# Performance work log

Measured on AMD Instinct MI355X. Metric: run time of the kernel, lower is better.

Reference implementation:

```python
import jax, jax.numpy as jnp
import numpy as np

# Model dims
B = 64            # scenes (memory batch)
APER = 16         # agents per scene (uniform `length`)
A = B * APER      # total agents = sum(length)
TPAST = 20
TFUT = 30         # len_future
C = 256           # controller_size
M = 128           # memory_m
N = 256           # memory_n
H = 5             # num_heads (future modes)
SPACE = N // APER # per-agent write slot band
EMB = 16
D = C + M         # decoder hidden size


def _gru(x, h, wih, whh, bih, bhh):
    """torch.nn.GRU single-cell step."""
    gi = x @ wih.T + bih
    gh = h @ whh.T + bhh
    ir, iz, inn = jnp.split(gi, 3, axis=-1)
    hr, hz, hn = jnp.split(gh, 3, axis=-1)
    r = jax.nn.sigmoid(ir + hr)
    z = jax.nn.sigmoid(iz + hz)
    n = jnp.tanh(inn + r * hn)
    return (1.0 - z) * n + z * h


def _address(k, beta, mem, mask):
    """NTM content addressing: beta-sharpened masked softmax over cosine sims.
    k: (...,B,APER,M), beta: (...,B,APER,1), mem: (B,N,M), mask: (APER,N)."""
    kn = k / (jnp.linalg.norm(k, axis=-1, keepdims=True) + 1e-16)
    mn = mem / (jnp.linalg.norm(mem, axis=-1, keepdims=True) + 1e-16)
    sim = jnp.einsum('...bam,bnm->...ban', kn, mn)
    logits = beta * sim + (mask - 1.0) * 1e9
    return jax.nn.softmax(logits, axis=-1)


def setup_inputs() -> dict:
    key = jax.random.key(0)
    ks = iter(jax.random.split(key, 64))
    def nrm(shape, scale):
        return jax.random.normal(next(ks), shape, dtype=jnp.float32) * scale
    inp = dict(
        past=nrm((A, TPAST, 2), 1.0),
        past_rel=nrm((A, TPAST, 2), 1.0),
        ep_w1=nrm((8, 2), 0.7), ep_b1=jnp.zeros(8), ep_w2=nrm((EMB, 8), 0.35), ep_b2=jnp.zeros(EMB),
        er_w1=nrm((8, 2), 0.7), er_b1=jnp.zeros(8), er_w2=nrm((EMB, 8), 0.35), er_b2=jnp.zeros(EMB),
        enc_wih=nrm((3 * C, EMB + M), 1.0 / np.sqrt(EMB + M)), enc_whh=nrm((3 * C, C), 1.0 / np.sqrt(C)),
        enc_bih=jnp.zeros(3 * C), enc_bhh=jnp.zeros(3 * C),
        rel_wih=nrm((3 * C, EMB), 1.0 / np.sqrt(EMB)), rel_whh=nrm((3 * C, C), 1.0 / np.sqrt(C)),
        rel_bih=jnp.zeros(3 * C), rel_bhh=jnp.zeros(3 * C),
        dec_wih=nrm((3 * D, D), 1.0 / np.sqrt(D)), dec_whh=nrm((3 * D, D), 1.0 / np.sqrt(D)),
        dec_bih=jnp.zeros(3 * D), dec_bhh=jnp.zeros(3 * D),
        out_w=nrm((2, D), 1.0 / np.sqrt(D)), out_b=jnp.zeros(2),
        read_w=nrm((H, M + 1, C), 1.0 / np.sqrt(C)), read_b=jnp.zeros((H, M + 1)),
        write_w=nrm((3 * M + 1, C), 1.0 / np.sqrt(C)), write_b=jnp.zeros(3 * M + 1),
        init_r=nrm((1, M), 0.01),
        h_bias=nrm((1, C), 0.05), h_rel_bias=nrm((1, C), 0.05), h_fut_bias=nrm((1, D), 0.05),
        mem_bias=nrm((N, M), 0.05),
    )
    return inp


def reference(past, past_rel, ep_w1, ep_b1, ep_w2, ep_b2, er_w1, er_b1, er_w2, er_b2,
              enc_wih, enc_whh, enc_bih, enc_bhh, rel_wih, rel_whh, rel_bih, rel_bhh,
              dec_wih, dec_whh, dec_bih, dec_bhh, out_w, out_b,
              read_w, read_b, write_w, write_b,
              init_r, h_bias, h_rel_bias, h_fut_bias, mem_bias):
    # Per-agent disjoint write bands; read mask = other agents' bands.
    owner = jnp.arange(N) // SPACE
    mask_w = (owner[None, :] == jnp.arange(APER)[:, None]).astype(jnp.float32)  # (APER,N)
    mask_r = 1.0 - mask_w

    def mlp(x, w1, b1, w2, b2):
        return jax.nn.relu(x @ w1.T + b1) @ w2.T + b2

    emb_p = jnp.transpose(mlp(past, ep_w1, ep_b1, ep_w2, ep_b2), (1, 0, 2))      # (T,A,16)
    emb_r = jnp.transpose(mlp(past_rel, er_w1, er_b1, er_w2, er_b2), (1, 0, 2))  # (T,A,16)

    def step(carry, xs):
        emb, embr = xs
        mem, h, hr, hf, r = carry
        h = _gru(jnp.concatenate([emb, r], axis=-1), h, enc_wih, enc_whh, enc_bih, enc_bhh)
        hr = _gru(embr, hr, rel_wih, rel_whh, rel_bih, rel_bhh)
        # write head: k, beta, erase, add
        wp = h @ write_w.T + write_b
        kw = jnp.tanh(wp[:, :M]).reshape(B, APER, M)
        betaw = jax.nn.softplus(wp[:, M:M + 1]).reshape(B, APER, 1)
        er = jax.nn.sigmoid(wp[:, M + 1:2 * M + 1]).reshape(B, APER, M)
        ad = jnp.tanh(wp[:, 2 * M + 1:]).reshape(B, APER, M)
        ww = _address(kw, betaw, mem, mask_w)                                    # (B,APER,N)
        # erase/add; write bands are disjoint across agents so aggregation is exact
        mem = mem * (1.0 - jnp.einsum('ban,bam->bnm', ww, er)) + jnp.einsum('ban,bam->bnm', ww, ad)
        # per-head reads
        rp = jnp.einsum('ac,hkc->hak', hr, read_w) + read_b[:, None, :]          # (H,A,M+1)
        kr = jnp.tanh(rp[..., :M]).reshape(H, B, APER, M)
        betar = jax.nn.softplus(rp[..., M:]).reshape(H, B, APER, 1)
        wr = _address(kr, betar, mem, mask_r)                                    # (H,B,APER,N)
        reads = jnp.einsum('hban,bnm->hbam', wr, mem).reshape(H, A, M)
        r = reads[0]
        # per-mode decoder
        dec_in = jnp.concatenate([jnp.broadcast_to(h[None], (H, A, C)), reads], axis=-1).reshape(H * A, D)
        hf = _gru(dec_in, hf, dec_wih, dec_whh, dec_bih, dec_bhh)
        out = (hf @ out_w.T + out_b).reshape(H, A, 2)
        return (mem, h, hr, hf, r), out

    carry0 = (jnp.broadcast_to(mem_bias[None], (B, N, M)),
              jnp.broadcast_to(h_bias, (A, C)),
              jnp.broadcast_to(h_rel_bias, (A, C)),
              jnp.broadcast_to(h_fut_bias, (H * A, D)),
              jnp.broadcast_to(init_r, (A, M)))
    carry, _ = jax.lax.scan(step, carry0, (emb_p, emb_r))
    zf = jnp.zeros((TFUT, A, EMB), dtype=past.dtype)
    carry, outs = jax.lax.scan(step, carry, (zf, zf))                            # (TFUT,H,A,2)
    pred_rel = jnp.transpose(outs, (2, 1, 0, 3))                                 # (A,H,TFUT,2)
    pred = past[:, -1][:, None, None, :] + jnp.cumsum(pred_rel, axis=2)
    return pred, pred_rel
```

## Files before the change

kernel.cpp:

```cpp
#include <hip/hip_runtime.h>
#include <math.h>

#define B_    64
#define APER_ 16
#define A_    1024
#define TPAST_ 20
#define TFUT_  30
#define C_    256
#define M_    128
#define N_    256
#define H_    5
#define EMB_  16
#define D_    384
#define TTOT_ 50

typedef short bf16x8 __attribute__((ext_vector_type(8)));
typedef float f32x4 __attribute__((ext_vector_type(4)));

__device__ __forceinline__ float sigmoidf_(float x) { return 1.0f / (1.0f + expf(-x)); }
__device__ __forceinline__ float softplusf_(float x) { return (x > 20.0f) ? x : log1pf(expf(x)); }
__device__ __forceinline__ unsigned short f2bf(float f) {
    unsigned u = __float_as_uint(f);
    return (unsigned short)((u + 0x7FFFu + ((u >> 16) & 1u)) >> 16);
}
__device__ __forceinline__ float bf2f(short s) {
    return __uint_as_float(((unsigned)(unsigned short)s) << 16);
}

struct Cvt { const float* src; short* dst; int rows, sk, dk, total; };
struct Cvt8 { Cvt c[8]; };

__global__ __launch_bounds__(256) void convert_all(Cvt8 p)
{
    const int stride = gridDim.x * 256;
    #pragma unroll
    for (int s = 0; s < 8; ++s) {
        const Cvt d = p.c[s];
        for (int idx = blockIdx.x * 256 + threadIdx.x; idx < d.total; idx += stride) {
            const int r = idx / d.dk, k = idx % d.dk;
            float v = (k < d.sk && r < d.rows) ? d.src[(size_t)r * d.sk + k] : 0.f;
            d.dst[idx] = (short)f2bf(v);
        }
    }
}

__global__ __launch_bounds__(256) void embed2_k(const float* __restrict__ past, const float* __restrict__ past_rel,
                                                const float* __restrict__ pw1, const float* __restrict__ pb1,
                                                const float* __restrict__ pw2, const float* __restrict__ pb2,
                                                const float* __restrict__ rw1, const float* __restrict__ rb1,
                                                const float* __restrict__ rw2, const float* __restrict__ rb2,
                                                short* __restrict__ emb_p, short* __restrict__ emb_r)
{
    const int idx0 = blockIdx.x * 256 + threadIdx.x;
    const int half = A_ * TPAST_;
    if (idx0 >= 2 * half) return;
    const bool second = idx0 >= half;
    const int idx = second ? idx0 - half : idx0;
    const float* x = second ? past_rel : past;
    const float* w1 = second ? rw1 : pw1; const float* b1 = second ? rb1 : pb1;
    const float* w2 = second ? rw2 : pw2; const float* b2 = second ? rb2 : pb2;
    short* emb = second ? emb_r : emb_p;

    const int a = idx / TPAST_, t = idx % TPAST_;
    const float x0 = x[(size_t)idx * 2], x1 = x[(size_t)idx * 2 + 1];
    float hbuf[8];
    #pragma unroll
    for (int j = 0; j < 8; ++j) hbuf[j] = fmaxf(0.f, w1[j * 2] * x0 + w1[j * 2 + 1] * x1 + b1[j]);
    short* e = emb + ((size_t)t * A_ + a) * EMB_;
    #pragma unroll
    for (int i = 0; i < 16; ++i) {
        float acc = b2[i];
        #pragma unroll
        for (int j = 0; j < 8; ++j) acc += w2[i * 8 + j] * hbuf[j];
        e[i] = (short)f2bf(acc);
    }
}

__global__ __launch_bounds__(256) void init_k(float* __restrict__ h, const float* __restrict__ h_bias, short* __restrict__ hb,
                                              float* __restrict__ hr, const float* __restrict__ hr_bias, short* __restrict__ hrb,
                                              const float* __restrict__ hf_bias, short* __restrict__ hfb,
                                              short* __restrict__ reads_b, const float* __restrict__ init_r,
                                              float* __restrict__ mem, short* __restrict__ memhi, short* __restrict__ memlo,
                                              float* __restrict__ normsG, const float* __restrict__ mem_bias)
{
    const int idx = blockIdx.x * 256 + threadIdx.x;
    if (idx < B_ * N_ * M_) {
        const float v = mem_bias[idx & (N_ * M_ - 1)];
        mem[idx] = v;
        const short hv = (short)f2bf(v);
        memhi[idx] = hv;
        memlo[idx] = (short)f2bf(v - bf2f(hv));
    }
    if (idx < B_ * N_) {
        const float* r = mem_bias + (size_t)(idx & (N_ - 1)) * M_;
        float ss = 0.f;
        for (int k = 0; k < M_; ++k) ss += r[k] * r[k];
        normsG[idx] = sqrtf(ss) + 1e-16f;
    }
    if (idx < A_ * C_) {
        float v = h_bias[idx & (C_ - 1)];
        h[idx] = v; hb[idx] = (short)f2bf(v);
        v = hr_bias[idx & (C_ - 1)];
        hr[idx] = v; hrb[idx] = (short)f2bf(v);
    }
    if (idx < H_ * A_ * D_) {
        hfb[idx] = (short)f2bf(hf_bias[idx % D_]);
    }
    if (idx < A_ * M_) reads_b[idx] = (short)f2bf(init_r[idx & (M_ - 1)]);
}

__device__ __forceinline__ void gru_tile_split(
    int role, float* __restrict__ xchLane,
    const short* __restrict__ X1, int K1,
    const short* __restrict__ X2, int K2,
    const short* __restrict__ Wih, int Kpad,
    const float* __restrict__ bih,
    const short* __restrict__ Hb, const short* __restrict__ Whh,
    const float* __restrict__ bhh,
    const float* __restrict__ Hprev,
    float* __restrict__ Hnew, short* __restrict__ Hnewb,
    int G, int rowBase, int colBase, int lane)
{
    const int l16 = lane & 15;
    const int kb8 = (lane >> 4) * 8;
    const f32x4 z4 = {0.f, 0.f, 0.f, 0.f};
    f32x4 a0[2][2], a1[2][2], a2[2][2];
    #pragma unroll
    for (int i = 0; i < 2; ++i)
        #pragma unroll
        for (int j = 0; j < 2; ++j) { a0[i][j] = z4; a1[i][j] = z4; a2[i][j] = z4; }

    if (role == 0) {
        for (int kc = 0; kc < Kpad; kc += 32) {
            const int k8 = kc + kb8;
            bf16x8 ax[2];
            #pragma unroll
            for (int i = 0; i < 2; ++i) {
                const int r = rowBase + i * 16 + l16;
                bf16x8 v = {0, 0, 0, 0, 0, 0, 0, 0};
                if (k8 < K1) {
                    if (X1) v = *(const bf16x8*)(X1 + (size_t)(r & 1023) * K1 + k8);
                } else if (k8 < K1 + K2) {
                    v = *(const bf16x8*)(X2 + (size_t)r * K2 + (k8 - K1));
                }
                ax[i] = v;
            }
            #pragma unroll
            for (int j = 0; j < 2; ++j) {
                const size_t wb = (size_t)(colBase + j * 16 + l16) * Kpad + k8;
                const bf16x8 b0 = *(const bf16x8*)(Wih + wb);
                const bf16x8 b1 = *(const bf16x8*)(Wih + (size_t)G * Kpad + wb);
                const bf16x8 b2 = *(const bf16x8*)(Wih + (size_t)2 * G * Kpad + wb);
                a0[0][j] = __builtin_amdgcn_mfma_f32_16x16x32_bf16(ax[0], b0, a0[0][j], 0, 0, 0);
                a0[1][j] = __builtin_amdgcn_mfma_f32_16x16x32_bf16(ax[1], b0, a0[1][j], 0, 0, 0);
                a1[0][j] = __builtin_amdgcn_mfma_f32_16x16x32_bf16(ax[0], b1, a1[0][j], 0, 0, 0);
                a1[1][j] = __builtin_amdgcn_mfma_f32_16x16x32_bf16(ax[1], b1, a1[1][j], 0, 0, 0);
                a2[0][j] = __builtin_amdgcn_mfma_f32_16x16x32_bf16(ax[0], b2, a2[0][j], 0, 0, 0);
                a2[1][j] = __builtin_amdgcn_mfma_f32_16x16x32_bf16(ax[1], b2, a2[1][j], 0, 0, 0);
            }
        }
        #pragma unroll
        for (int i = 0; i < 2; ++i)
            #pragma unroll
            for (int j = 0; j < 2; ++j)
                #pragma unroll
                for (int q = 0; q < 4; ++q) {
                    const int base = (i * 2 + j) * 4 + q;
                    xchLane[base]      = a0[i][j][q];
                    xchLane[16 + base] = a1[i][j][q];
                    xchLane[32 + base] = a2[i][j][q];
                }
    } else {
        for (int kc = 0; kc < G; kc += 32) {
            const int k8 = kc + kb8;
            bf16x8 ah[2];
            #pragma unroll
            for (int i = 0; i < 2; ++i)
                ah[i] = *(const bf16x8*)(Hb + (size_t)(rowBase + i * 16 + l16) * G + k8);
            #pragma unroll
            for (int j = 0; j < 2; ++j) {
                const size_t wb = (size_t)(colBase + j * 16 + l16) * G + k8;
                const bf16x8 b0 = *(const bf16x8*)(Whh + wb);
                const bf16x8 b1 = *(const bf16x8*)(Whh + (size_t)G * G + wb);
                const bf16x8 b2 = *(const bf16x8*)(Whh + (size_t)2 * G * G + wb);
                a0[0][j] = __builtin_amdgcn_mfma_f32_16x16x32_bf16(ah[0], b0, a0[0][j], 0, 0, 0);
                a0[1][j] = __builtin_amdgcn_mfma_f32_16x16x32_bf16(ah[1], b0, a0[1][j], 0, 0, 0);
                a1[0][j] = __builtin_amdgcn_mfma_f32_16x16x32_bf16(ah[0], b1, a1[0][j], 0, 0, 0);
                a1[1][j] = __builtin_amdgcn_mfma_f32_16x16x32_bf16(ah[1], b1, a1[1][j], 0, 0, 0);
                a2[0][j] = __builtin_amdgcn_mfma_f32_16x16x32_bf16(ah[0], b2, a2[0][j], 0, 0, 0);
                a2[1][j] = __builtin_amdgcn_mfma_f32_16x16x32_bf16(ah[1], b2, a2[1][j], 0, 0, 0);
            }
        }
    }
    __syncthreads();
    if (role != 1) return;

    const int r4 = (lane >> 4) * 4;
    #pragma unroll
    for (int j = 0; j < 2; ++j) {
        const int col = colBase + j * 16 + l16;
        const float b0c = bih[col] + bhh[col];
        const float b1c = bih[G + col] + bhh[G + col];
        const float bi2 = bih[2 * G + col], bh2 = bhh[2 * G + col];
        #pragma unroll
        for (int i = 0; i < 2; ++i) {
            #pragma unroll
            for (int q = 0; q < 4; ++q) {
                const int row = rowBase + i * 16 + r4 + q;
                const int base = (i * 2 + j) * 4 + q;
                const float arv = a0[i][j][q] + xchLane[base];
                const float azv = a1[i][j][q] + xchLane[16 + base];
                const float aniv = xchLane[32 + base];
                const float anhv = a2[i][j][q];
                const float rr = sigmoidf_(arv + b0c);
                const float zz = sigmoidf_(azv + b1c);
                const float nn = tanhf(aniv + bi2 + rr * (anhv + bh2));
                const float hp = Hprev ? Hprev[(size_t)row * G + col]
                                       : bf2f(Hb[(size_t)row * G + col]);
                const float hv = (1.f - zz) * nn + zz * hp;
                if (Hnew) Hnew[(size_t)row * G + col] = hv;
                Hnewb[(size_t)row * G + col] = (short)f2bf(hv);
            }
        }
    }
}

__device__ __forceinline__ void gemm_tile(
    const short* __restrict__ Xb, const short* __restrict__ Wb,
    const float* __restrict__ bias, float* __restrict__ Out,
    int Ncols, int K, int rowBase, int colBase, int lane)
{
    const int l16 = lane & 15;
    const int kb8 = (lane >> 4) * 8;
    const f32x4 z4 = {0.f, 0.f, 0.f, 0.f};
    f32x4 acc[2][2] = {{z4, z4}, {z4, z4}};

    for (int kc = 0; kc < K; kc += 32) {
        const int k8 = kc + kb8;
        const bf16x8 a0 = *(const bf16x8*)(Xb + (size_t)(rowBase + l16) * K + k8);
        const bf16x8 a1 = *(const bf16x8*)(Xb + (size_t)(rowBase + 16 + l16) * K + k8);
        const bf16x8 b0 = *(const bf16x8*)(Wb + (size_t)(colBase + l16) * K + k8);
        const bf16x8 b1 = *(const bf16x8*)(Wb + (size_t)(colBase + 16 + l16) * K + k8);
        acc[0][0] = __builtin_amdgcn_mfma_f32_16x16x32_bf16(a0, b0, acc[0][0], 0, 0, 0);
        acc[0][1] = __builtin_amdgcn_mfma_f32_16x16x32_bf16(a0, b1, acc[0][1], 0, 0, 0);
        acc[1][0] = __builtin_amdgcn_mfma_f32_16x16x32_bf16(a1, b0, acc[1][0], 0, 0, 0);
        acc[1][1] = __builtin_amdgcn_mfma_f32_16x16x32_bf16(a1, b1, acc[1][1], 0, 0, 0);
    }
    const int r4 = (lane >> 4) * 4;
    #pragma unroll
    for (int j = 0; j < 2; ++j) {
        const int col = colBase + j * 16 + l16;
        if (col >= Ncols) continue;
        const float bv = bias[col];
        #pragma unroll
        for (int i = 0; i < 2; ++i)
            #pragma unroll
            for (int q = 0; q < 4; ++q) {
                const int row = rowBase + i * 16 + r4 + q;
                Out[(size_t)row * Ncols + col] = acc[i][j][q] + bv;
            }
    }
}

__global__ __launch_bounds__(256) void phaseA(
    const short* __restrict__ ep, const short* __restrict__ er,
    const short* __restrict__ enc_wih, const float* __restrict__ enc_bih,
    const short* __restrict__ enc_whh, const float* __restrict__ enc_bhh,
    const short* __restrict__ rel_wih, const float* __restrict__ rel_bih,
    const short* __restrict__ rel_whh, const float* __restrict__ rel_bhh,
    const short* __restrict__ dec_wih, const float* __restrict__ dec_bih,
    const short* __restrict__ dec_whh, const float* __restrict__ dec_bhh,
    const float* __restrict__ hc, const short* __restrict__ hbc,
    float* __restrict__ hn, short* __restrict__ hbn,
    const float* __restrict__ hrc, const short* __restrict__ hrbc,
    float* __restrict__ hrn, short* __restrict__ hrbn,
    const short* __restrict__ hfbc, short* __restrict__ hfbn,
    const short* __restrict__ reads_b,
    int decBlocks, int encBlocks)
{
    __shared__ float xch[2][64][49];
    const int bid = blockIdx.x;
    const int wv = threadIdx.x >> 6;
    const int lane = threadIdx.x & 63;
    const int pair = wv >> 1, role = wv & 1;
    float* xchLane = &xch[pair][lane][0];

    if (bid < decBlocks) {
        const int tile = bid * 2 + pair;
        gru_tile_split(role, xchLane,
                       hbc, 256, reads_b, 128, dec_wih, 384, dec_bih,
                       hfbc, dec_whh, dec_bhh, nullptr, nullptr, hfbn, D_,
                       (tile / 12) * 32, (tile % 12) * 32, lane);
    } else if (bid < decBlocks + encBlocks) {
        const int tile = (bid - decBlocks) * 2 + pair;
        gru_tile_split(role, xchLane,
                       ep, 16, reads_b, 128, enc_wih, 160, enc_bih,
                       hbc, enc_whh, enc_bhh, hc, hn, hbn, C_,
                       (tile >> 3) * 32, (tile & 7) * 32, lane);
    } else {
        const int tile = (bid - decBlocks - encBlocks) * 2 + pair;
        gru_tile_split(role, xchLane,
                       er, 16, nullptr, 0, rel_wih, 32, rel_bih,
                       hrbc, rel_whh, rel_bhh, hrc, hrn, hrbn, C_,
                       (tile >> 3) * 32, (tile & 7) * 32, lane);
    }
}

__global__ __launch_bounds__(256) void phaseHeads(
    const short* __restrict__ hbn, const short* __restrict__ write_w_b,
    const float* __restrict__ write_b, float* __restrict__ wp,
    const short* __restrict__ hrbn, const short* __restrict__ read_w_b,
    const float* __restrict__ read_b, float* __restrict__ rp,
    const short* __restrict__ hfbn, const float* __restrict__ out_w,
    const float* __restrict__ out_b, float* __restrict__ predrel,
    int outT, int wpBlocks, int rpBlocks)
{
    const int bid = blockIdx.x;
    const int wave = threadIdx.x >> 6;
    const int lane = threadIdx.x & 63;

    if (bid < wpBlocks) {
        const int tile = bid * 4 + wave;
        gemm_tile(hbn, write_w_b, write_b, wp, 385, C_,
                  (tile & 31) * 32, (tile >> 5) * 32, lane);
    } else if (bid < wpBlocks + rpBlocks) {
        const int tile = (bid - wpBlocks) * 4 + wave;
        gemm_tile(hrbn, read_w_b, read_b, rp, 645, C_,
                  (tile & 31) * 32, (tile >> 5) * 32, lane);
    } else {
        const int widx = (bid - wpBlocks - rpBlocks) * 4 + wave;
        const int g = lane >> 3, li = lane & 7;
        const int row = widx * 8 + g;
        const short* hrow = hfbn + (size_t)row * D_;
        float a0 = 0.f, a1 = 0.f;
        #pragma unroll
        for (int u = 0; u < 6; ++u) {
            const int k0 = u * 64 + li * 8;
            const bf16x8 v = *(const bf16x8*)(hrow + k0);
            #pragma unroll
            for (int r = 0; r < 8; ++r) {
                const float f = bf2f(v[r]);
                a0 = fmaf(f, out_w[k0 + r], a0);
                a1 = fmaf(f, out_w[D_ + k0 + r], a1);
            }
        }
        a0 += __shfl_xor(a0, 1); a0 += __shfl_xor(a0, 2); a0 += __shfl_xor(a0, 4);
        a1 += __shfl_xor(a1, 1); a1 += __shfl_xor(a1, 2); a1 += __shfl_xor(a1, 4);
        if (li == 0) {
            const int hh = row >> 10, aa = row & 1023;
            float* o = predrel + (((size_t)aa * H_ + hh) * TFUT_ + outT) * 2;
            o[0] = a0 + out_b[0];
            o[1] = a1 + out_b[1];
        }
    }
}

__global__ __launch_bounds__(256) void write_mem_k(const float* __restrict__ wp,
                                                   float* __restrict__ mem,
                                                   short* __restrict__ memhi, short* __restrict__ memlo,
                                                   float* __restrict__ normsG)
{
    const int a = blockIdx.x;
    const int b = a >> 4, p = a & 15;
    __shared__ float kw[128], er[128], ad[128], red[256], ww[16], logit[16];
    __shared__ float buf[2048];
    __shared__ float beta_s, knorm_s;
    const int tid = threadIdx.x;
    const float* w = wp + (size_t)a * 385;
    if (tid < 128) {
        kw[tid] = tanhf(w[tid]);
        er[tid] = sigmoidf_(w[129 + tid]);
        ad[tid] = tanhf(w[257 + tid]);
    }
    if (tid == 0) beta_s = softplusf_(w[128]);
    __syncthreads();

    red[tid] = (tid < 128) ? kw[tid] * kw[tid] : 0.f;
    __syncthreads();
    for (int s = 128; s > 0; s >>= 1) { if (tid < s) red[tid] += red[tid + s]; __syncthreads(); }
    if (tid == 0) knorm_s = sqrtf(red[0]) + 1e-16f;
    __syncthreads();

    const int s = tid >> 4, j = tid & 15;
    float dot = 0.f, ss = 0.f;
    {
        const float* mrow = mem + ((size_t)(b * N_) + p * 16 + s) * M_;
        for (int k = j; k < 128; k += 16) { float v = mrow[k]; dot += kw[k] * v; ss += v * v; }
    }
    red[tid] = dot; __syncthreads();
    for (int st = 8; st > 0; st >>= 1) { if (j < st) red[tid] += red[tid + st]; __syncthreads(); }
    float dotf = red[s * 16];
    __syncthreads();
    red[tid] = ss; __syncthreads();
    for (int st = 8; st > 0; st >>= 1) { if (j < st) red[tid] += red[tid + st]; __syncthreads(); }
    float ssf = red[s * 16];
    if (j == 0) {
        float mn = sqrtf(ssf) + 1e-16f;
        logit[s] = beta_s * (dotf / (mn * knorm_s));
    }
    __syncthreads();
    if (tid == 0) {
        float mx = -1e30f;
        for (int i = 0; i < 16; ++i) mx = fmaxf(mx, logit[i]);
        float sum = 0.f;
        for (int i = 0; i < 16; ++i) { float e = __expf(logit[i] - mx); ww[i] = e; sum += e; }
        float inv = 1.f / sum;
        for (int i = 0; i < 16; ++i) ww[i] *= inv;
    }
    __syncthreads();
    for (int idx = tid; idx < 16 * 128; idx += 256) {
        int si = idx >> 7, m = idx & 127;
        size_t g = ((size_t)(b * N_) + p * 16 + si) * M_ + m;
        float wwv = ww[si];
        float v = mem[g] * (1.f - wwv * er[m]) + wwv * ad[m];
        mem[g] = v;
        const short hv = (short)f2bf(v);
        memhi[g] = hv;
        memlo[g] = (short)f2bf(v - bf2f(hv));
        buf[idx] = v;
    }
    __syncthreads();
    {
        float ssq = 0.f;
        #pragma unroll
        for (int i = 0; i < 8; ++i) { float v = buf[s * 128 + j + 16 * i]; ssq += v * v; }
        #pragma unroll
        for (int m = 1; m < 16; m <<= 1) ssq += __shfl_xor(ssq, m);
        if (j == 0) normsG[b * N_ + p * 16 + s] = sqrtf(ssq) + 1e-16f;
    }
}

__global__ __launch_bounds__(256) void read_k2(const float* __restrict__ rp,
                                               const float* __restrict__ mem,
                                               const short* __restrict__ memhi,
                                               const short* __restrict__ memlo,
                                               const float* __restrict__ normsG,
                                               short* __restrict__ reads_b)
{
    const int b = blockIdx.x;
    const int h = blockIdx.y;
    __shared__ __align__(16) float kq[16 * 132];
    __shared__ float S[16 * 260];
    __shared__ float beta_s[16], knorm_s[16], inv_s[16];
    const int t = threadIdx.x;
    const int a = t >> 4;
    const int sub = t & 15;

    {
        const float* base = rp + ((size_t)(b * 16 + a)) * 645 + h * 129;
        const int k0 = sub * 8;
        float v[8]; float ss = 0.f;
        #pragma unroll
        for (int r = 0; r < 8; ++r) { v[r] = tanhf(base[k0 + r]); ss += v[r] * v[r]; }
        float* dst = kq + a * 132 + k0;
        *(float4*)dst = make_float4(v[0], v[1], v[2], v[3]);
        *(float4*)(dst + 4) = make_float4(v[4], v[5], v[6], v[7]);
        #pragma unroll
        for (int m = 1; m < 16; m <<= 1) ss += __shfl_xor(ss, m);
        if (sub == 0) {
            knorm_s[a] = sqrtf(ss) + 1e-16f;
            beta_s[a] = softplusf_(base[128]);
        }
    }
    __syncthreads();

    {
        const int wave = t >> 6, lane = t & 63;
        const int l16 = lane & 15, kb8 = (lane >> 4) * 8;
        const int slotBase = wave * 64;
        const f32x4 z4 = {0.f, 0.f, 0.f, 0.f};
        f32x4 acc[4] = {z4, z4, z4, z4};
        const short* mbh = memhi + (size_t)b * N_ * M_;
        const short* mbl = memlo + (size_t)b * N_ * M_;
        #pragma unroll
        for (int kc = 0; kc < 128; kc += 32) {
            const float* ap = kq + l16 * 132 + kc + kb8;
            bf16x8 ah, al;
            #pragma unroll
            for (int r = 0; r < 8; ++r) {
                const float av = ap[r];
                const short hv = (short)f2bf(av);
                ah[r] = hv; al[r] = (short)f2bf(av - bf2f(hv));
            }
            #pragma unroll
            for (int tt = 0; tt < 4; ++tt) {
                const size_t roff = (size_t)(slotBase + tt * 16 + l16) * M_ + kc + kb8;
                const bf16x8 bh = *(const bf16x8*)(mbh + roff);
                const bf16x8 bl = *(const bf16x8*)(mbl + roff);
                acc[tt] = __builtin_amdgcn_mfma_f32_16x16x32_bf16(ah, bh, acc[tt], 0, 0, 0);
                acc[tt] = __builtin_amdgcn_mfma_f32_16x16x32_bf16(ah, bl, acc[tt], 0, 0, 0);
                acc[tt] = __builtin_amdgcn_mfma_f32_16x16x32_bf16(al, bh, acc[tt], 0, 0, 0);
            }
        }
        const int r4 = (lane >> 4) * 4;
        #pragma unroll
        for (int tt = 0; tt < 4; ++tt) {
            const int slot = slotBase + tt * 16 + l16;
            const float nv = normsG[b * N_ + slot];
            #pragma unroll
            for (int q = 0; q < 4; ++q) {
                const int aq = r4 + q;
                const float lg = ((slot >> 4) == aq) ? -1e30f
                               : beta_s[aq] * acc[tt][q] / (nv * knorm_s[aq]);
                S[aq * 260 + slot] = lg;
            }
        }
    }
    __syncthreads();

    {
        float mx = -1e30f;
        #pragma unroll
        for (int i = 0; i < 16; ++i) mx = fmaxf(mx, S[a * 260 + sub + 16 * i]);
        #pragma unroll
        for (int m = 1; m < 16; m <<= 1) mx = fmaxf(mx, __shfl_xor(mx, m));
        float e[16]; float sum = 0.f;
        #pragma unroll
        for (int i = 0; i < 16; ++i) { e[i] = __expf(S[a * 260 + sub + 16 * i] - mx); sum += e[i]; }
        #pragma unroll
        for (int i = 0; i < 16; ++i) S[a * 260 + sub + 16 * i] = e[i];
        #pragma unroll
        for (int m = 1; m < 16; m <<= 1) sum += __shfl_xor(sum, m);
        if (sub == 0) inv_s[a] = 1.f / sum;
    }
    __syncthreads();

    {
        const int m0 = sub * 8;
        const float* mb = mem + (size_t)b * N_ * M_ + m0;
        float acc[8];
        #pragma unroll
        for (int r = 0; r < 8; ++r) acc[r] = 0.f;
        const float* Sa = S + a * 260;
        #pragma unroll 4
        for (int n = 0; n < N_; ++n) {
            const float w = Sa[n];
            const float4 v0 = *(const float4*)(mb + (size_t)n * M_);
            const float4 v1 = *(const float4*)(mb + (size_t)n * M_ + 4);
            acc[0] = fmaf(w, v0.x, acc[0]); acc[1] = fmaf(w, v0.y, acc[1]);
            acc[2] = fmaf(w, v0.z, acc[2]); acc[3] = fmaf(w, v0.w, acc[3]);
            acc[4] = fmaf(w, v1.x, acc[4]); acc[5] = fmaf(w, v1.y, acc[5]);
            acc[6] = fmaf(w, v1.z, acc[6]); acc[7] = fmaf(w, v1.w, acc[7]);
        }
        const float inv = inv_s[a];
        short pk[8];
        #pragma unroll
        for (int r = 0; r < 8; ++r) pk[r] = (short)f2bf(acc[r] * inv);
        *(bf16x8*)(reads_b + ((size_t)h * A_ + b * 16 + a) * M_ + m0) = *(bf16x8*)pk;
    }
}

__global__ __launch_bounds__(256) void cumsum_k(const float* __restrict__ past,
                                                const float* __restrict__ predrel,
                                                float* __restrict__ pred)
{
    const int idx = blockIdx.x * 256 + threadIdx.x;
    if (idx >= A_ * H_ * 2) return;
    const int c = idx & 1;
    const int ah = idx >> 1;
    const int a = ah / H_;
    float acc = past[((size_t)a * TPAST_ + TPAST_ - 1) * 2 + c];
    const float* pr = predrel + (size_t)ah * TFUT_ * 2 + c;
    float* pd = pred + (size_t)ah * TFUT_ * 2 + c;
    for (int t = 0; t < TFUT_; ++t) { acc += pr[t * 2]; pd[t * 2] = acc; }
}

extern "C" void kernel_launch(void* const* d_in, const int* in_sizes, int n_in,
                              void* d_out, int out_size, void* d_ws, size_t ws_size,
                              hipStream_t stream)
{
    const float* past       = (const float*)d_in[0];
    const float* past_rel   = (const float*)d_in[1];
    const float* ep_w1      = (const float*)d_in[2];
    const float* ep_b1      = (const float*)d_in[3];
    const float* ep_w2      = (const float*)d_in[4];
    const float* ep_b2      = (const float*)d_in[5];
    const float* er_w1      = (const float*)d_in[6];
    const float* er_b1      = (const float*)d_in[7];
    const float* er_w2      = (const float*)d_in[8];
    const float* er_b2      = (const float*)d_in[9];
    const float* enc_wih    = (const float*)d_in[10];
    const float* enc_whh    = (const float*)d_in[11];
    const float* enc_bih    = (const float*)d_in[12];
    const float* enc_bhh    = (const float*)d_in[13];
    const float* rel_wih    = (const float*)d_in[14];
    const float* rel_whh    = (const float*)d_in[15];
    const float* rel_bih    = (const float*)d_in[16];
    const float* rel_bhh    = (const float*)d_in[17];
    const float* dec_wih    = (const float*)d_in[18];
    const float* dec_whh    = (const float*)d_in[19];
    const float* dec_bih    = (const float*)d_in[20];
    const float* dec_bhh    = (const float*)d_in[21];
    const float* out_w      = (const float*)d_in[22];
    const float* out_b      = (const float*)d_in[23];
    const float* read_w     = (const float*)d_in[24];
    const float* read_b     = (const float*)d_in[25];
    const float* write_w    = (const float*)d_in[26];
    const float* write_b    = (const float*)d_in[27];
    const float* init_r     = (const float*)d_in[28];
    const float* h_bias     = (const float*)d_in[29];
    const float* h_rel_bias = (const float*)d_in[30];
    const float* h_fut_bias = (const float*)d_in[31];
    const float* mem_bias   = (const float*)d_in[32];

    float* pred    = (float*)d_out;
    float* predrel = pred + (size_t)A_ * H_ * TFUT_ * 2;

    float* ws = (float*)d_ws;
    size_t off = 0;
    auto alloc = [&](size_t n) { float* p = ws + off; off += n; return p; };
    float* h0     = alloc((size_t)A_ * C_);
    float* h1     = alloc((size_t)A_ * C_);
    float* hr0    = alloc((size_t)A_ * C_);
    float* hr1    = alloc((size_t)A_ * C_);
    float* mem    = alloc((size_t)B_ * N_ * M_);
    float* wp     = alloc((size_t)A_ * 385);
    float* rp     = alloc((size_t)A_ * 645);
    float* normsG = alloc((size_t)B_ * N_);

    short* sws = (short*)(ws + off);
    size_t soff = 0;
    auto salloc = [&](size_t n) { short* p = sws + soff; soff += n; return p; };
    short* emb_p_b   = salloc((size_t)TPAST_ * A_ * EMB_);
    short* emb_r_b   = salloc((size_t)TPAST_ * A_ * EMB_);
    short* hb0       = salloc((size_t)A_ * C_);
    short* hb1       = salloc((size_t)A_ * C_);
    short* hrb0      = salloc((size_t)A_ * C_);
    short* hrb1      = salloc((size_t)A_ * C_);
    short* hfb0      = salloc((size_t)H_ * A_ * D_);
    short* hfb1      = salloc((size_t)H_ * A_ * D_);
    short* reads_b   = salloc((size_t)H_ * A_ * M_);
    short* memhi     = salloc((size_t)B_ * N_ * M_);
    short* memlo     = salloc((size_t)B_ * N_ * M_);
    short* enc_wih_b = salloc((size_t)768 * 160);
    short* enc_whh_b = salloc((size_t)768 * 256);
    short* rel_wih_b = salloc((size_t)768 * 32);
    short* rel_whh_b = salloc((size_t)768 * 256);
    short* dec_wih_b = salloc((size_t)1152 * 384);
    short* dec_whh_b = salloc((size_t)1152 * 384);
    short* write_w_b = salloc((size_t)416 * 256);
    short* read_w_b  = salloc((size_t)672 * 256);
    (void)ws_size; (void)in_sizes; (void)n_in; (void)out_size;

    Cvt8 cp;
    cp.c[0] = {enc_wih, enc_wih_b, 768, 144, 160, 768 * 160};
    cp.c[1] = {enc_whh, enc_whh_b, 768, 256, 256, 768 * 256};
    cp.c[2] = {rel_wih, rel_wih_b, 768, 16, 32, 768 * 32};
    cp.c[3] = {rel_whh, rel_whh_b, 768, 256, 256, 768 * 256};
    cp.c[4] = {dec_wih, dec_wih_b, 1152, 384, 384, 1152 * 384};
    cp.c[5] = {dec_whh, dec_whh_b, 1152, 384, 384, 1152 * 384};
    cp.c[6] = {write_w, write_w_b, 385, 256, 256, 416 * 256};
    cp.c[7] = {read_w, read_w_b, 645, 256, 256, 672 * 256};
    convert_all<<<1024, 256, 0, stream>>>(cp);

    init_k<<<(B_ * N_ * M_ + 255) / 256, 256, 0, stream>>>(
        h0, h_bias, hb0, hr0, h_rel_bias, hrb0, h_fut_bias, hfb0,
        reads_b, init_r, mem, memhi, memlo, normsG, mem_bias);
    embed2_k<<<(2 * A_ * TPAST_ + 255) / 256, 256, 0, stream>>>(
        past, past_rel, ep_w1, ep_b1, ep_w2, ep_b2, er_w1, er_b1, er_w2, er_b2,
        emb_p_b, emb_r_b);

    float *hc = h0, *hn = h1, *hrc = hr0, *hrn = hr1;
    short *hbc = hb0, *hbn = hb1, *hrbc = hrb0, *hrbn = hrb1, *hfbc = hfb0, *hfbn = hfb1;

    const dim3 g_read(B_, H_);

    for (int t = 0; t < TTOT_; ++t) {
        const short* ep = (t < TPAST_) ? emb_p_b + (size_t)t * A_ * EMB_ : nullptr;
        const short* er = (t < TPAST_) ? emb_r_b + (size_t)t * A_ * EMB_ : nullptr;

        const int decBlocks = (t == 0) ? 0 : 960;
        phaseA<<<decBlocks + 256, 256, 0, stream>>>(
            ep, er,
            enc_wih_b, enc_bih, enc_whh_b, enc_bhh,
            rel_wih_b, rel_bih, rel_whh_b, rel_bhh,
            dec_wih_b, dec_bih, dec_whh_b, dec_bhh,
            hc, hbc, hn, hbn,
            hrc, hrbc, hrn, hrbn,
            hfbc, hfbn,
            reads_b, decBlocks, 128);

        const int gridH = (t >= 21) ? 432 : 272;
        phaseHeads<<<gridH, 256, 0, stream>>>(
            hbn, write_w_b, write_b, wp,
            hrbn, read_w_b, read_b, rp,
            hfbn, out_w, out_b, predrel, t - 21, 104, 168);

        write_mem_k<<<A_, 256, 0, stream>>>(wp, mem, memhi, memlo, normsG);

        read_k2<<<g_read, 256, 0, stream>>>(rp, mem, memhi, memlo, normsG, reads_b);

        float* tf; short* ts;
        tf = hc; hc = hn; hn = tf;       ts = hbc; hbc = hbn; hbn = ts;
        tf = hrc; hrc = hrn; hrn = tf;   ts = hrbc; hrbc = hrbn; hrbn = ts;
        if (t >= 1) {
            ts = hfbc; hfbc = hfbn; hfbn = ts;
        }
    }

    phaseA<<<960, 256, 0, stream>>>(
        nullptr, nullptr,
        enc_wih_b, enc_bih, enc_whh_b, enc_bhh,
        rel_wih_b, rel_bih, rel_whh_b, rel_bhh,
        dec_wih_b, dec_bih, dec_whh_b, dec_bhh,
        hc, hbc, hn, hbn,
        hrc, hrbc, hrn, hrbn,
        hfbc, hfbn,
        reads_b, 960, 0);
    phaseHeads<<<160, 256, 0, stream>>>(
        hbn, write_w_b, write_b, wp,
        hrbn, read_w_b, read_b, rp,
        hfbn, out_w, out_b, predrel, TFUT_ - 1, 0, 0);
    cumsum_k<<<(A_ * H_ * 2 + 255) / 256, 256, 0, stream>>>(past, predrel, pred);
}
```

Measured before the change: 6.146 ms.

## Fuse write-projection GEMM with memory write and drop fp32 memory copy

The write-head projection GEMM is folded into the memory-write step. Each of 64 per-scene blocks computes its 16 agents' write parameters into shared memory with MFMA, then applies the addressing softmax and erase/add update in place. The separate fp32 memory array is removed, and the hi/lo bf16 split pair becomes the only memory representation, read by both the write and read kernels. This removes one launch per step, the wp global round trip and the fp32 memory traffic. In exchange, the fused part runs on only 64 blocks with large shared-memory use, and values are reconstructed from the bf16 pairs on every access.

Result: slower. 6.653 ms (+8.2%).

```diff
diff --git a/kernel.cpp b/kernel.cpp
--- a/kernel.cpp
+++ b/kernel.cpp
@@ -80,13 +80,12 @@
                                               float* __restrict__ hr, const float* __restrict__ hr_bias, short* __restrict__ hrb,
                                               const float* __restrict__ hf_bias, short* __restrict__ hfb,
                                               short* __restrict__ reads_b, const float* __restrict__ init_r,
-                                              float* __restrict__ mem, short* __restrict__ memhi, short* __restrict__ memlo,
+                                              short* __restrict__ memhi, short* __restrict__ memlo,
                                               float* __restrict__ normsG, const float* __restrict__ mem_bias)
 {
     const int idx = blockIdx.x * 256 + threadIdx.x;
     if (idx < B_ * N_ * M_) {
         const float v = mem_bias[idx & (N_ * M_ - 1)];
-        mem[idx] = v;
         const short hv = (short)f2bf(v);
         memhi[idx] = hv;
         memlo[idx] = (short)f2bf(v - bf2f(hv));
@@ -306,29 +305,124 @@
     }
 }
 
-__global__ __launch_bounds__(256) void phaseHeads(
+__global__ __launch_bounds__(256) void phaseB(
     const short* __restrict__ hbn, const short* __restrict__ write_w_b,
-    const float* __restrict__ write_b, float* __restrict__ wp,
+    const float* __restrict__ write_b,
+    short* __restrict__ memhi, short* __restrict__ memlo,
+    float* __restrict__ normsG,
     const short* __restrict__ hrbn, const short* __restrict__ read_w_b,
     const float* __restrict__ read_b, float* __restrict__ rp,
     const short* __restrict__ hfbn, const float* __restrict__ out_w,
     const float* __restrict__ out_b, float* __restrict__ predrel,
-    int outT, int wpBlocks, int rpBlocks)
-{
+    int outT, int wrBlocks, int rpBlocks)
+{
+    __shared__ float wpL[16][420];
+    __shared__ float kwL[16][132], erL[16][132], adL[16][132];
+    __shared__ float betaL[16];
     const int bid = blockIdx.x;
-    const int wave = threadIdx.x >> 6;
-    const int lane = threadIdx.x & 63;
-
-    if (bid < wpBlocks) {
-        const int tile = bid * 4 + wave;
-        gemm_tile(hbn, write_w_b, write_b, wp, 385, C_,
-                  (tile & 31) * 32, (tile >> 5) * 32, lane);
-    } else if (bid < wpBlocks + rpBlocks) {
-        const int tile = (bid - wpBlocks) * 4 + wave;
+    const int tid = threadIdx.x;
+    const int wave = tid >> 6;
+    const int lane = tid & 63;
+
+    if (bid < wrBlocks) {
+        const int b = bid;
+        const int l16 = lane & 15;
+        const int kb8 = (lane >> 4) * 8;
+        const f32x4 z4 = {0.f, 0.f, 0.f, 0.f};
+
+        #pragma unroll
+        for (int ti = 0; ti < 4; ++ti) {
+            const int tile = wave * 4 + ti;
+            if (tile >= 13) break;
+            const int colBase = tile * 32;
+            f32x4 acc[2] = {z4, z4};
+            for (int kc = 0; kc < 256; kc += 32) {
+                const int k8 = kc + kb8;
+                const bf16x8 av = *(const bf16x8*)(hbn + (size_t)(b * 16 + l16) * C_ + k8);
+                const bf16x8 b0 = *(const bf16x8*)(write_w_b + (size_t)(colBase + l16) * C_ + k8);
+                const bf16x8 b1 = *(const bf16x8*)(write_w_b + (size_t)(colBase + 16 + l16) * C_ + k8);
+                acc[0] = __builtin_amdgcn_mfma_f32_16x16x32_bf16(av, b0, acc[0], 0, 0, 0);
+                acc[1] = __builtin_amdgcn_mfma_f32_16x16x32_bf16(av, b1, acc[1], 0, 0, 0);
+            }
+            const int r4 = (lane >> 4) * 4;
+            #pragma unroll
+            for (int j = 0; j < 2; ++j) {
+                const int col = colBase + j * 16 + l16;
+                if (col >= 385) continue;
+                #pragma unroll
+                for (int q = 0; q < 4; ++q)
+                    wpL[r4 + q][col] = acc[j][q] + write_b[col];
+            }
+        }
+        __syncthreads();
+
+        for (int idx = tid; idx < 2048; idx += 256) {
+            const int a2 = idx >> 7, k = idx & 127;
+            kwL[a2][k] = tanhf(wpL[a2][k]);
+            erL[a2][k] = sigmoidf_(wpL[a2][129 + k]);
+            adL[a2][k] = tanhf(wpL[a2][257 + k]);
+        }
+        if (tid < 16) betaL[tid] = softplusf_(wpL[tid][128]);
+        __syncthreads();
+
+        const int a = tid >> 4, s = tid & 15;
+        float kss = 0.f;
+        #pragma unroll
+        for (int i = 0; i < 8; ++i) { const float v = kwL[a][s * 8 + i]; kss += v * v; }
+        #pragma unroll
+        for (int m = 1; m < 16; m <<= 1) kss += __shfl_xor(kss, m);
+        const float knorm = sqrtf(kss) + 1e-16f;
+
+        const size_t row = (size_t)(b * N_) + a * 16 + s;
+        const short* hi = memhi + row * M_;
+        const short* lo = memlo + row * M_;
+        float dot = 0.f, ss = 0.f;
+        for (int k8 = 0; k8 < 128; k8 += 8) {
+            const bf16x8 vh = *(const bf16x8*)(hi + k8);
+            const bf16x8 vl = *(const bf16x8*)(lo + k8);
+            #pragma unroll
+            for (int r = 0; r < 8; ++r) {
+                const float v = bf2f(vh[r]) + bf2f(vl[r]);
+                dot = fmaf(kwL[a][k8 + r], v, dot);
+                ss = fmaf(v, v, ss);
+            }
+        }
+        const float logit = betaL[a] * (dot / ((sqrtf(ss) + 1e-16f) * knorm));
+        float mx = logit;
+        #pragma unroll
+        for (int m = 1; m < 16; m <<= 1) mx = fmaxf(mx, __shfl_xor(mx, m));
+        const float e = __expf(logit - mx);
+        float sum = e;
+        #pragma unroll
+        for (int m = 1; m < 16; m <<= 1) sum += __shfl_xor(sum, m);
+        const float ww = e / sum;
+
+        float ssq = 0.f;
+        short* hiw = memhi + row * M_;
+        short* low = memlo + row * M_;
+        for (int k8 = 0; k8 < 128; k8 += 8) {
+            const bf16x8 vh = *(const bf16x8*)(hi + k8);
+            const bf16x8 vl = *(const bf16x8*)(lo + k8);
+            bf16x8 oh, ol;
+            #pragma unroll
+            for (int r = 0; r < 8; ++r) {
+                const float old = bf2f(vh[r]) + bf2f(vl[r]);
+                const float v = old * (1.f - ww * erL[a][k8 + r]) + ww * adL[a][k8 + r];
+                const short hv = (short)f2bf(v);
+                oh[r] = hv;
+                ol[r] = (short)f2bf(v - bf2f(hv));
+                ssq = fmaf(v, v, ssq);
+            }
+            *(bf16x8*)(hiw + k8) = oh;
+            *(bf16x8*)(low + k8) = ol;
+        }
+        normsG[row] = sqrtf(ssq) + 1e-16f;
+    } else if (bid < wrBlocks + rpBlocks) {
+        const int tile = (bid - wrBlocks) * 4 + wave;
         gemm_tile(hrbn, read_w_b, read_b, rp, 645, C_,
                   (tile & 31) * 32, (tile >> 5) * 32, lane);
     } else {
-        const int widx = (bid - wpBlocks - rpBlocks) * 4 + wave;
+        const int widx = (bid - wrBlocks - rpBlocks) * 4 + wave;
         const int g = lane >> 3, li = lane & 7;
         const int row = widx * 8 + g;
         const short* hrow = hfbn + (size_t)row * D_;
@@ -355,83 +449,7 @@
     }
 }
 
-__global__ __launch_bounds__(256) void write_mem_k(const float* __restrict__ wp,
-                                                   float* __restrict__ mem,
-                                                   short* __restrict__ memhi, short* __restrict__ memlo,
-                                                   float* __restrict__ normsG)
-{
-    const int a = blockIdx.x;
-    const int b = a >> 4, p = a & 15;
-    __shared__ float kw[128], er[128], ad[128], red[256], ww[16], logit[16];
-    __shared__ float buf[2048];
-    __shared__ float beta_s, knorm_s;
-    const int tid = threadIdx.x;
-    const float* w = wp + (size_t)a * 385;
-    if (tid < 128) {
-        kw[tid] = tanhf(w[tid]);
-        er[tid] = sigmoidf_(w[129 + tid]);
-        ad[tid] = tanhf(w[257 + tid]);
-    }
-    if (tid == 0) beta_s = softplusf_(w[128]);
-    __syncthreads();
-
-    red[tid] = (tid < 128) ? kw[tid] * kw[tid] : 0.f;
-    __syncthreads();
-    for (int s = 128; s > 0; s >>= 1) { if (tid < s) red[tid] += red[tid + s]; __syncthreads(); }
-    if (tid == 0) knorm_s = sqrtf(red[0]) + 1e-16f;
-    __syncthreads();
-
-    const int s = tid >> 4, j = tid & 15;
-    float dot = 0.f, ss = 0.f;
-    {
-        const float* mrow = mem + ((size_t)(b * N_) + p * 16 + s) * M_;
-        for (int k = j; k < 128; k += 16) { float v = mrow[k]; dot += kw[k] * v; ss += v * v; }
-    }
-    red[tid] = dot; __syncthreads();
-    for (int st = 8; st > 0; st >>= 1) { if (j < st) red[tid] += red[tid + st]; __syncthreads(); }
-    float dotf = red[s * 16];
-    __syncthreads();
-    red[tid] = ss; __syncthreads();
-    for (int st = 8; st > 0; st >>= 1) { if (j < st) red[tid] += red[tid + st]; __syncthreads(); }
-    float ssf = red[s * 16];
-    if (j == 0) {
-        float mn = sqrtf(ssf) + 1e-16f;
-        logit[s] = beta_s * (dotf / (mn * knorm_s));
-    }
-    __syncthreads();
-    if (tid == 0) {
-        float mx = -1e30f;
-        for (int i = 0; i < 16; ++i) mx = fmaxf(mx, logit[i]);
-        float sum = 0.f;
-        for (int i = 0; i < 16; ++i) { float e = __expf(logit[i] - mx); ww[i] = e; sum += e; }
-        float inv = 1.f / sum;
-        for (int i = 0; i < 16; ++i) ww[i] *= inv;
-    }
-    __syncthreads();
-    for (int idx = tid; idx < 16 * 128; idx += 256) {
-        int si = idx >> 7, m = idx & 127;
-        size_t g = ((size_t)(b * N_) + p * 16 + si) * M_ + m;
-        float wwv = ww[si];
-        float v = mem[g] * (1.f - wwv * er[m]) + wwv * ad[m];
-        mem[g] = v;
-        const short hv = (short)f2bf(v);
-        memhi[g] = hv;
-        memlo[g] = (short)f2bf(v - bf2f(hv));
-        buf[idx] = v;
-    }
-    __syncthreads();
-    {
-        float ssq = 0.f;
-        #pragma unroll
-        for (int i = 0; i < 8; ++i) { float v = buf[s * 128 + j + 16 * i]; ssq += v * v; }
-        #pragma unroll
-        for (int m = 1; m < 16; m <<= 1) ssq += __shfl_xor(ssq, m);
-        if (j == 0) normsG[b * N_ + p * 16 + s] = sqrtf(ssq) + 1e-16f;
-    }
-}
-
 __global__ __launch_bounds__(256) void read_k2(const float* __restrict__ rp,
-                                               const float* __restrict__ mem,
                                                const short* __restrict__ memhi,
                                                const short* __restrict__ memlo,
                                                const float* __restrict__ normsG,
@@ -527,20 +545,20 @@
 
     {
         const int m0 = sub * 8;
-        const float* mb = mem + (size_t)b * N_ * M_ + m0;
+        const short* mbh = memhi + (size_t)b * N_ * M_ + m0;
+        const short* mbl = memlo + (size_t)b * N_ * M_ + m0;
         float acc[8];
         #pragma unroll
         for (int r = 0; r < 8; ++r) acc[r] = 0.f;
         const float* Sa = S + a * 260;
-        #pragma unroll 4
+        #pragma unroll 2
         for (int n = 0; n < N_; ++n) {
             const float w = Sa[n];
-            const float4 v0 = *(const float4*)(mb + (size_t)n * M_);
-            const float4 v1 = *(const float4*)(mb + (size_t)n * M_ + 4);
-            acc[0] = fmaf(w, v0.x, acc[0]); acc[1] = fmaf(w, v0.y, acc[1]);
-            acc[2] = fmaf(w, v0.z, acc[2]); acc[3] = fmaf(w, v0.w, acc[3]);
-            acc[4] = fmaf(w, v1.x, acc[4]); acc[5] = fmaf(w, v1.y, acc[5]);
-            acc[6] = fmaf(w, v1.z, acc[6]); acc[7] = fmaf(w, v1.w, acc[7]);
+            const bf16x8 vh = *(const bf16x8*)(mbh + (size_t)n * M_);
+            const bf16x8 vl = *(const bf16x8*)(mbl + (size_t)n * M_);
+            #pragma unroll
+            for (int r = 0; r < 8; ++r)
+                acc[r] = fmaf(w, bf2f(vh[r]) + bf2f(vl[r]), acc[r]);
         }
         const float inv = inv_s[a];
         short pk[8];
@@ -613,8 +631,6 @@
     float* h1     = alloc((size_t)A_ * C_);
     float* hr0    = alloc((size_t)A_ * C_);
     float* hr1    = alloc((size_t)A_ * C_);
-    float* mem    = alloc((size_t)B_ * N_ * M_);
-    float* wp     = alloc((size_t)A_ * 385);
     float* rp     = alloc((size_t)A_ * 645);
     float* normsG = alloc((size_t)B_ * N_);
 
@@ -655,7 +671,7 @@
 
     init_k<<<(B_ * N_ * M_ + 255) / 256, 256, 0, stream>>>(
         h0, h_bias, hb0, hr0, h_rel_bias, hrb0, h_fut_bias, hfb0,
-        reads_b, init_r, mem, memhi, memlo, normsG, mem_bias);
+        reads_b, init_r, memhi, memlo, normsG, mem_bias);
     embed2_k<<<(2 * A_ * TPAST_ + 255) / 256, 256, 0, stream>>>(
         past, past_rel, ep_w1, ep_b1, ep_w2, ep_b2, er_w1, er_b1, er_w2, er_b2,
         emb_p_b, emb_r_b);
@@ -680,15 +696,13 @@
             hfbc, hfbn,
             reads_b, decBlocks, 128);
 
-        const int gridH = (t >= 21) ? 432 : 272;
-        phaseHeads<<<gridH, 256, 0, stream>>>(
-            hbn, write_w_b, write_b, wp,
+        const int gridB = (t >= 21) ? 392 : 232;
+        phaseB<<<gridB, 256, 0, stream>>>(
+            hbn, write_w_b, write_b, memhi, memlo, normsG,
             hrbn, read_w_b, read_b, rp,
-            hfbn, out_w, out_b, predrel, t - 21, 104, 168);
-
-        write_mem_k<<<A_, 256, 0, stream>>>(wp, mem, memhi, memlo, normsG);
-
-        read_k2<<<g_read, 256, 0, stream>>>(rp, mem, memhi, memlo, normsG, reads_b);
+            hfbn, out_w, out_b, predrel, t - 21, 64, 168);
+
+        read_k2<<<g_read, 256, 0, stream>>>(rp, memhi, memlo, normsG, reads_b);
 
         float* tf; short* ts;
         tf = hc; hc = hn; hn = tf;       ts = hbc; hbc = hbn; hbn = ts;
@@ -707,8 +721,8 @@
         hrc, hrbc, hrn, hrbn,
         hfbc, hfbn,
         reads_b, 960, 0);
-    phaseHeads<<<160, 256, 0, stream>>>(
-        hbn, write_w_b, write_b, wp,
+    phaseB<<<160, 256, 0, stream>>>(
+        hbn, write_w_b, write_b, memhi, memlo, normsG,
         hrbn, read_w_b, read_b, rp,
         hfbn, out_w, out_b, predrel, TFUT_ - 1, 0, 0);
     cumsum_k<<<(A_ * H_ * 2 + 255) / 256, 256, 0, stream>>>(past, predrel, pred);
```
